# Optimization experiments

Measured on AMD Instinct MI355X. Metric: run time of the kernel, lower is better.

## Reference

```python
import jax, jax.numpy as jnp
import numpy as np

# static config (mirrors init_kwargs)
F_T, S = 8, 24            # video_shape = (F_T, S, S)
K, DIL = 3, 1             # kernel_size, dilation (same for all 3 axes)
HEADS, DHEAD, DIM = 8, 64, 512
INNER = HEADS * DHEAD
PAD = DIL * (K - 1)       # causal: pad 2 at the FRONT of each spatial axis
KJ = K ** 3               # 27 neighbors per query
N_VID = F_T * S * S       # 4608 video tokens


def causal_pad(t):
    # t: [B, D, F, S, S] -> pad front of f/h/w axes (torch F.pad (PAD*?,0) causal layout)
    return jnp.pad(t, ((0, 0), (0, 0), (PAD, 0), (PAD, 0), (PAD, 0)))


def unfold3d(t):
    # torch unfoldNd equivalent. t: [B, D, F+PAD, S+PAD, S+PAD]
    # returns [B, N_VID, KJ, D]; kernel offsets ordered (kf, kh, kw) w fastest,
    # matching torch unfold's channel-major / kernel-minor layout after the
    # rearrange 'b (d j) i -> b i j d'.
    sl = []
    for i in range(K):
        for j in range(K):
            for kk in range(K):
                sl.append(t[:, :, i * DIL:i * DIL + F_T,
                                  j * DIL:j * DIL + S,
                                  kk * DIL:kk * DIL + S])
    u = jnp.stack(sl, axis=2)                      # [B, D, KJ, F, S, S]
    B, D = t.shape[0], t.shape[1]
    u = u.reshape(B, D, KJ, N_VID)
    return jnp.transpose(u, (0, 3, 2, 1))          # [B, N_VID, KJ, D]


def make_mask():
    # True where the neighbor falls into zero padding (out-of-range / future under causal pad)
    ones = jnp.ones((1, 1, F_T, S, S), jnp.float32)
    u = unfold3d(causal_pad(ones))[0, :, :, 0]     # [N_VID, KJ]
    m = u == 0.0
    return jnp.pad(m, ((0, 0), (1, 0)), constant_values=False)  # bos col never masked


def stable_softmax(t, alpha=32.0 ** 2):
    t = t / alpha
    t = t - jax.lax.stop_gradient(jnp.max(t, axis=-1, keepdims=True))
    return jax.nn.softmax(t * alpha, axis=-1)


def setup_inputs() -> dict:
    key = jax.random.key(0)
    ks = jax.random.split(key, 9)
    return {
        "x": jax.random.normal(ks[0], (1, N_VID + 1, DIM), jnp.float32),
        "Wq": jax.random.normal(ks[1], (DIM, INNER), jnp.float32) * 0.02,
        "Wkv": jax.random.normal(ks[2], (DIM, 2 * INNER), jnp.float32) * 0.02,
        "W_th": jax.random.normal(ks[3], (HEADS, HEADS), jnp.float32) * 0.2,
        "Wout": jax.random.normal(ks[4], (INNER, DIM), jnp.float32) * 0.02,
        "bout": jax.random.normal(ks[5], (DIM,), jnp.float32) * 0.02,
        "ax1": jax.random.normal(ks[6], (K, HEADS), jnp.float32),
        "ax2": jax.random.normal(ks[7], (K, HEADS), jnp.float32),
        "ax3": jax.random.normal(ks[8], (K, HEADS), jnp.float32),
    }


def reference(x, Wq, Wkv, W_th, Wout, bout, ax1, ax2, ax3):
    b, n, _ = x.shape                       # b=1, n = 1 + N_VID (no extra padding)
    h, d = HEADS, DHEAD
    scale = d ** -0.5

    q = x @ Wq
    k, v = jnp.split(x @ Wkv, 2, axis=-1)

    def to_heads(t):  # 'b n (h d) -> (b h) n d'
        return t.reshape(b, n, h, d).transpose(0, 2, 1, 3).reshape(b * h, n, d)

    q, k, v = map(to_heads, (q, k, v))
    q = q[:, 1:] * scale                    # drop bos query
    k_bos, v_bos = k[:, :1], v[:, :1]       # [bh, 1, d]
    k, v = k[:, 1:], v[:, 1:]

    def to_vid(t):  # 'b (f h w) d -> b d f h w'
        return t.reshape(b * h, F_T, S, S, d).transpose(0, 4, 1, 2, 3)

    ku = unfold3d(causal_pad(to_vid(k)))    # [bh, N, KJ, d]
    vu = unfold3d(causal_pad(to_vid(v)))
    N = ku.shape[1]

    kb = jnp.broadcast_to(k_bos[:, :, None, :], (b * h, N, 1, d))
    vb = jnp.broadcast_to(v_bos[:, :, None, :], (b * h, N, 1, d))
    ku = jnp.concatenate([kb, ku], axis=2)  # [bh, N, KJ+1, d]
    vu = jnp.concatenate([vb, vu], axis=2)

    sim = jnp.einsum('bid,bijd->bij', q, ku)                 # [bh, N, KJ+1]

    # axial relative position bias over the 3x3x3 kernel, pad 0 for bos column
    rel = (ax1[:, None, None, :] + ax2[None, :, None, :] + ax3[None, None, :, :])
    rel = rel.reshape(KJ, h)                                 # [27, h]
    bias = jnp.pad(rel.T[:, None, :], ((0, 0), (0, 0), (1, 0)))  # [h, 1, KJ+1]

    sim = sim.reshape(b, h, N, KJ + 1) + bias[None]
    mask = make_mask()                                       # [N, KJ+1]
    sim = jnp.where(mask[None, None], -jnp.finfo(sim.dtype).max, sim)

    attn = stable_softmax(sim)                               # [b, h, N, KJ+1]
    attn = jnp.einsum('hg,bgij->bhij', W_th, attn)           # talking heads 1x1 conv

    out = jnp.einsum('bhij,bhijd->bhid', attn, vu.reshape(b, h, N, KJ + 1, d))
    out = jnp.concatenate([v_bos.reshape(b, h, 1, d), out], axis=2)  # re-attach bos value
    out = out.transpose(0, 2, 1, 3).reshape(b, n, h * d)     # '(b h) n d -> b n (h d)'
    return out @ Wout + bout
```

## Files before the change

### kernel.cpp

```cpp
#include <hip/hip_runtime.h>
#include <hip/hip_bf16.h>


constexpr int TFR   = 8;
constexpr int SDIM  = 24;
constexpr int NVID  = TFR * SDIM * SDIM;
constexpr int NTOK  = NVID + 1;
constexpr int NH    = 8;
constexpr int DM    = 512;
constexpr int NJ    = 28;

typedef __attribute__((ext_vector_type(8))) short bf16x8;
typedef __attribute__((ext_vector_type(8))) unsigned short ushort8;
typedef __attribute__((ext_vector_type(4))) float f32x4;

typedef const __attribute__((address_space(1))) unsigned int* gas_ptr;
typedef __attribute__((address_space(3))) unsigned int* las_ptr;

__device__ __forceinline__ float bf2f(unsigned short u) {
    return __uint_as_float((unsigned)u << 16);
}
__device__ __forceinline__ unsigned short f2bf(float f) {
    __hip_bfloat16 h = __float2bfloat16(f);
    return reinterpret_cast<unsigned short&>(h);
}

__global__ __launch_bounds__(256)
void prep_w(const float* __restrict__ Wq, const float* __restrict__ Wkv,
            const float* __restrict__ Wout, const float* __restrict__ x,
            __hip_bfloat16* __restrict__ Wqkvt, __hip_bfloat16* __restrict__ Woutt,
            __hip_bfloat16* __restrict__ xb)
{
    const int tid = threadIdx.x;
    int tb = blockIdx.x;

    if (tb >= 1024) {
        const size_t base = (size_t)(tb - 1024) * 2048 + (size_t)tid * 8;
        if (base < (size_t)NTOK * DM) {
            const float4 f0 = *(const float4*)(x + base);
            const float4 f1 = *(const float4*)(x + base + 4);
            unsigned short v[8] = { f2bf(f0.x), f2bf(f0.y), f2bf(f0.z), f2bf(f0.w),
                                    f2bf(f1.x), f2bf(f1.y), f2bf(f1.z), f2bf(f1.w) };
            *(ushort8*)(xb + base) = *(const ushort8*)v;
        }
        return;
    }

    __shared__ float t[32][33];
    const float* W; __hip_bfloat16* Wt; int Nd, tX, rowOff;
    if (tb < 256)      { W = Wq;   Wt = Wqkvt; Nd = 512;  tX = 16; rowOff = 0;   }
    else if (tb < 768) { tb -= 256; W = Wkv;  Wt = Wqkvt; Nd = 1024; tX = 32; rowOff = 512; }
    else               { tb -= 768; W = Wout; Wt = Woutt; Nd = 512;  tX = 16; rowOff = 0;   }
    const int n0 = (tb % tX) * 32, k0 = (tb / tX) * 32;
    const int r  = tid >> 3;
    const int c4 = (tid & 7) * 4;
    const float4 v = *(const float4*)(W + (size_t)(k0 + r) * Nd + n0 + c4);
    t[r][c4 + 0] = v.x; t[r][c4 + 1] = v.y; t[r][c4 + 2] = v.z; t[r][c4 + 3] = v.w;
    __syncthreads();
    #pragma unroll
    for (int j = 0; j < 4; ++j)
        Wt[(size_t)(rowOff + n0 + r) * 512 + k0 + c4 + j] = __float2bfloat16(t[c4 + j][r]);
}

__global__ __launch_bounds__(256)
void gemm_qkv(const __hip_bfloat16* __restrict__ Ab, const __hip_bfloat16* __restrict__ Bt,
              float* __restrict__ Cq, __hip_bfloat16* __restrict__ Ckv, int M)
{
    constexpr int BM = 128, BN = 128, BK = 64, K = 512;
    __shared__ __align__(16) short As[2][BM * BK];
    __shared__ __align__(16) short Bs[2][BN * BK];

    const int tid  = threadIdx.x;
    const int bid  = blockIdx.x;
    const int xcd  = bid & 7, pos = bid >> 3;
    const int L    = (xcd < 4) ? xcd * 56 + pos : 224 + (xcd - 4) * 55 + pos;
    const int m0   = (L / 12) * BM;
    const int n0   = (L % 12) * BN;

    const int lane = tid & 63;
    const int wave = tid >> 6;
    const int wm   = (wave >> 1) * 64;
    const int wn   = (wave & 1) * 64;
    const int col  = lane & 15;
    const int quad = lane >> 4;

    f32x4 acc[4][4] = {};

    auto stage = [&](int buf, int k0) {
        #pragma unroll
        for (int it = 0; it < 4; ++it) {
            const int idx = it * 256 + tid;
            const int r   = idx >> 3;
            const int u   = (idx & 7) ^ (r & 7);
            const int gm  = (m0 + r < M) ? (m0 + r) : (M - 1);
            const __hip_bfloat16* gp = Ab + (size_t)gm * K + k0 + u * 8;
            __builtin_amdgcn_global_load_lds(
                (gas_ptr)gp, (las_ptr)&As[buf][(it * 256 + wave * 64) * 8], 16, 0, 0);
        }
        #pragma unroll
        for (int it = 0; it < 4; ++it) {
            const int idx = it * 256 + tid;
            const int r   = idx >> 3;
            const int u   = (idx & 7) ^ (r & 7);
            const __hip_bfloat16* gp = Bt + (size_t)(n0 + r) * K + k0 + u * 8;
            __builtin_amdgcn_global_load_lds(
                (gas_ptr)gp, (las_ptr)&Bs[buf][(it * 256 + wave * 64) * 8], 16, 0, 0);
        }
    };

    stage(0, 0);

    #pragma unroll
    for (int t = 0; t < K / BK; ++t) {
        const int cur = t & 1;
        if (t + 1 < K / BK) {
            stage(cur ^ 1, (t + 1) * BK);
            asm volatile("s_waitcnt vmcnt(8)" ::: "memory");
        } else {
            asm volatile("s_waitcnt vmcnt(0)" ::: "memory");
        }
        __builtin_amdgcn_s_barrier();

        #pragma unroll
        for (int ks = 0; ks < 2; ++ks) {
            bf16x8 af[4], bfr[4];
            #pragma unroll
            for (int mt = 0; mt < 4; ++mt) {
                const int r = wm + mt * 16 + col;
                const int u = (ks * 4 + quad) ^ (r & 7);
                af[mt] = *(const bf16x8*)(&As[cur][r * BK + u * 8]);
            }
            #pragma unroll
            for (int nt = 0; nt < 4; ++nt) {
                const int r = wn + nt * 16 + col;
                const int u = (ks * 4 + quad) ^ (r & 7);
                bfr[nt] = *(const bf16x8*)(&Bs[cur][r * BK + u * 8]);
            }
            #pragma unroll
            for (int mt = 0; mt < 4; ++mt)
                #pragma unroll
                for (int nt = 0; nt < 4; ++nt)
                    acc[mt][nt] = __builtin_amdgcn_mfma_f32_16x16x32_bf16(
                        af[mt], bfr[nt], acc[mt][nt], 0, 0, 0);
        }
        __builtin_amdgcn_s_barrier();
    }

    const bool isQ = (n0 < 512);
    #pragma unroll
    for (int mt = 0; mt < 4; ++mt) {
        #pragma unroll
        for (int r = 0; r < 4; ++r) {
            const int row = m0 + wm + mt * 16 + quad * 4 + r;
            if (row >= M) continue;
            #pragma unroll
            for (int nt = 0; nt < 4; ++nt) {
                const int cg = n0 + wn + nt * 16 + col;
                const float v = acc[mt][nt][r];
                if (isQ) Cq[(size_t)row * 512 + cg] = v * 0.125f;
                else     Ckv[(size_t)row * 1024 + (cg - 512)] = __float2bfloat16(v);
            }
        }
    }
}

__global__ __launch_bounds__(256)
void gemm_out(const __hip_bfloat16* __restrict__ A, const __hip_bfloat16* __restrict__ Bt,
              float* __restrict__ C, int M, const float* __restrict__ bias)
{
    constexpr int BM = 64, BN = 64, BK = 64, K = 512;
    __shared__ __align__(16) short As[2][BM * BK];
    __shared__ __align__(16) short Bs[2][BN * BK];

    const int tid  = threadIdx.x;
    const int bid  = blockIdx.x;
    const int L    = (bid & 7) * 73 + (bid >> 3);
    const int m0   = (L >> 3) * BM;
    const int n0   = (L & 7) * BN;
    const int lane = tid & 63;
    const int wave = tid >> 6;
    const int wm   = (wave >> 1) * 32;
    const int wn   = (wave & 1) * 32;
    const int col  = lane & 15;
    const int quad = lane >> 4;

    f32x4 acc[2][2] = {};

    auto stage = [&](int buf, int k0) {
        #pragma unroll
        for (int it = 0; it < 2; ++it) {
            const int idx = it * 256 + tid;
            const int r   = idx >> 3;
            const int u   = (idx & 7) ^ (r & 7);
            const int gm  = (m0 + r < M) ? (m0 + r) : (M - 1);
            const __hip_bfloat16* gp = A + (size_t)gm * K + k0 + u * 8;
            __builtin_amdgcn_global_load_lds(
                (gas_ptr)gp, (las_ptr)&As[buf][(it * 256 + wave * 64) * 8], 16, 0, 0);
        }
        #pragma unroll
        for (int it = 0; it < 2; ++it) {
            const int idx = it * 256 + tid;
            const int r   = idx >> 3;
            const int u   = (idx & 7) ^ (r & 7);
            const __hip_bfloat16* gp = Bt + (size_t)(n0 + r) * K + k0 + u * 8;
            __builtin_amdgcn_global_load_lds(
                (gas_ptr)gp, (las_ptr)&Bs[buf][(it * 256 + wave * 64) * 8], 16, 0, 0);
        }
    };

    stage(0, 0);

    #pragma unroll
    for (int t = 0; t < K / BK; ++t) {
        const int cur = t & 1;
        if (t + 1 < K / BK) {
            stage(cur ^ 1, (t + 1) * BK);
            asm volatile("s_waitcnt vmcnt(4)" ::: "memory");
        } else {
            asm volatile("s_waitcnt vmcnt(0)" ::: "memory");
        }
        __builtin_amdgcn_s_barrier();

        #pragma unroll
        for (int ks = 0; ks < 2; ++ks) {
            bf16x8 af[2], bfr[2];
            #pragma unroll
            for (int mt = 0; mt < 2; ++mt) {
                const int r = wm + mt * 16 + col;
                const int u = (ks * 4 + quad) ^ (r & 7);
                af[mt] = *(const bf16x8*)(&As[cur][r * BK + u * 8]);
            }
            #pragma unroll
            for (int nt = 0; nt < 2; ++nt) {
                const int r = wn + nt * 16 + col;
                const int u = (ks * 4 + quad) ^ (r & 7);
                bfr[nt] = *(const bf16x8*)(&Bs[cur][r * BK + u * 8]);
            }
            #pragma unroll
            for (int mt = 0; mt < 2; ++mt)
                #pragma unroll
                for (int nt = 0; nt < 2; ++nt)
                    acc[mt][nt] = __builtin_amdgcn_mfma_f32_16x16x32_bf16(
                        af[mt], bfr[nt], acc[mt][nt], 0, 0, 0);
        }
        __builtin_amdgcn_s_barrier();
    }

    #pragma unroll
    for (int mt = 0; mt < 2; ++mt) {
        #pragma unroll
        for (int r = 0; r < 4; ++r) {
            const int row = m0 + wm + mt * 16 + quad * 4 + r;
            if (row >= M) continue;
            #pragma unroll
            for (int nt = 0; nt < 2; ++nt) {
                const int cg = n0 + wn + nt * 16 + col;
                C[(size_t)row * 512 + cg] = acc[mt][nt][r] + bias[cg];
            }
        }
    }
}

__device__ __forceinline__ void neigh(int j, int t, int y, int x,
                                      int& row, bool& val,
                                      int& di, int& dj, int& dk)
{
    if (j == 0) { row = 0; val = true; di = 0; dj = 0; dk = 0; return; }
    const int jp = j - 1;
    di = jp / 9; dj = (jp / 3) % 3; dk = jp % 3;
    const int tt = t + di - 2, yy = y + dj - 2, xx = x + dk - 2;
    val = (tt >= 0) && (yy >= 0) && (xx >= 0);
    row = val ? 1 + tt * SDIM * SDIM + yy * SDIM + xx : 0;
}

#define ISSUE_K(B, DST)                                                     \
    { _Pragma("unroll")                                                     \
      for (int u = 0; u < 7; ++u) {                                         \
        int row; bool val; int di, dj, dk;                                  \
        neigh((B) * 7 + u, t, y, x, row, val, di, dj, dk);                  \
        DST[u] = *(const ushort8*)(KVb + (size_t)row * 1024 + lane * 8);    \
      } }

#define DOTS_K(B, SRC)                                                      \
    { _Pragma("unroll")                                                     \
      for (int u = 0; u < 7; ++u) {                                         \
        const int j = (B) * 7 + u;                                          \
        int row; bool val; int di, dj, dk;                                  \
        neigh(j, t, y, x, row, val, di, dj, dk);                            \
        float p = 0.f;                                                      \
        _Pragma("unroll")                                                   \
        for (int e = 0; e < 8; ++e) p += bf2f(SRC[u][e]) * qf[e];           \
        p += __shfl_xor(p, 1);                                              \
        p += __shfl_xor(p, 2);                                              \
        p += __shfl_xor(p, 4);                                              \
        sim[j] = !val ? -1e30f                                              \
               : (j == 0 ? p : p + a1[di] + a2[dj] + a3[dk]);               \
      } }

#define ISSUE_V(B, DST)                                                     \
    { _Pragma("unroll")                                                     \
      for (int u = 0; u < 7; ++u) {                                         \
        int row; bool val; int di, dj, dk;                                  \
        neigh((B) * 7 + u, t, y, x, row, val, di, dj, dk);                  \
        DST[u] = *(const ushort8*)(KVb + (size_t)row * 1024 + 512 + lane * 8); \
      } }

#define ACC_V(B, SRC)                                                       \
    { _Pragma("unroll")                                                     \
      for (int u = 0; u < 7; ++u) {                                         \
        const int j = (B) * 7 + u;                                          \
        const float w = mixed_s[wave][g * NJ + j];                          \
        _Pragma("unroll")                                                   \
        for (int e = 0; e < 8; ++e) acc8[e] += w * bf2f(SRC[u][e]);         \
      } }

__global__ __launch_bounds__(256, 3)
void attn_v5(const float* __restrict__ Q, const __hip_bfloat16* __restrict__ KVb,
             __hip_bfloat16* __restrict__ O,
             const float* __restrict__ W_th,
             const float* __restrict__ ax1, const float* __restrict__ ax2,
             const float* __restrict__ ax3)
{
    __shared__ float attn_s[4][NH * NJ];
    __shared__ float mixed_s[4][NH * NJ];

    const int tid  = threadIdx.x;
    const int wave = tid >> 6;
    const int lane = tid & 63;
    const int g    = lane >> 3;
    const int s    = lane & 7;
    const int bsw  = (blockIdx.x & 7) * (NVID / 4 / 8) + (blockIdx.x >> 3);
    const int i    = __builtin_amdgcn_readfirstlane(bsw * 4 + wave);
    const int qrow = i + 1;

    const int t  = i / (SDIM * SDIM);
    const int rm = i % (SDIM * SDIM);
    const int y  = rm / SDIM;
    const int x  = rm % SDIM;

    float qf[8];
    {
        const float4 q0 = *(const float4*)(Q + (size_t)qrow * DM + lane * 8);
        const float4 q1 = *(const float4*)(Q + (size_t)qrow * DM + lane * 8 + 4);
        qf[0] = q0.x; qf[1] = q0.y; qf[2] = q0.z; qf[3] = q0.w;
        qf[4] = q1.x; qf[5] = q1.y; qf[6] = q1.z; qf[7] = q1.w;
    }
    float a1[3], a2[3], a3[3];
    #pragma unroll
    for (int d = 0; d < 3; ++d) {
        a1[d] = ax1[d * NH + g];
        a2[d] = ax2[d * NH + g];
        a3[d] = ax3[d * NH + g];
    }

    float sim[NJ];
    ushort8 bufA[7], bufB[7];
    ISSUE_K(0, bufA);
    ISSUE_K(1, bufB);
    DOTS_K(0, bufA);
    ISSUE_K(2, bufA);
    DOTS_K(1, bufB);
    ISSUE_K(3, bufB);
    DOTS_K(2, bufA);
    DOTS_K(3, bufB);

    ISSUE_V(0, bufA);

    float m = -1e30f;
    #pragma unroll
    for (int j = 0; j < NJ; ++j) m = fmaxf(m, sim[j]);
    float ssum = 0.f;
    #pragma unroll
    for (int j = 0; j < NJ; ++j) { sim[j] = __expf(sim[j] - m); ssum += sim[j]; }
    const float inv = 1.f / ssum;
    #pragma unroll
    for (int j = 0; j < NJ; ++j) sim[j] *= inv;

    if (s == 0) {
        #pragma unroll
        for (int u = 0; u < 7; ++u) {
            f32x4 v4 = { sim[4*u], sim[4*u+1], sim[4*u+2], sim[4*u+3] };
            *(f32x4*)(&attn_s[wave][g * NJ + 4 * u]) = v4;
        }
    }
    asm volatile("s_waitcnt lgkmcnt(0)" ::: "memory");
    __builtin_amdgcn_s_barrier();

    if (tid < NH * NJ) {
        const int h = tid / NJ, j = tid % NJ;
        #pragma unroll
        for (int q = 0; q < 4; ++q) {
            float acc = 0.f;
            #pragma unroll
            for (int gg = 0; gg < NH; ++gg)
                acc += W_th[h * NH + gg] * attn_s[q][gg * NJ + j];
            mixed_s[q][h * NJ + j] = acc;
        }
    }
    asm volatile("s_waitcnt lgkmcnt(0)" ::: "memory");
    __builtin_amdgcn_s_barrier();

    float acc8[8] = {};
    ISSUE_V(1, bufB);
    ACC_V(0, bufA);
    ISSUE_V(2, bufA);
    ACC_V(1, bufB);
    ISSUE_V(3, bufB);
    ACC_V(2, bufA);
    ACC_V(3, bufB);

    unsigned short o[8];
    #pragma unroll
    for (int e = 0; e < 8; ++e) o[e] = f2bf(acc8[e]);
    *(ushort8*)(O + (size_t)qrow * DM + lane * 8) = *(const ushort8*)o;

    if (i == 0) {
        const ushort8 vb0 = *(const ushort8*)(KVb + 512 + lane * 8);
        *(ushort8*)(O + lane * 8) = vb0;
    }
}

extern "C" void kernel_launch(void* const* d_in, const int* in_sizes, int n_in,
                              void* d_out, int out_size, void* d_ws, size_t ws_size,
                              hipStream_t stream)
{
    const float* x    = (const float*)d_in[0];
    const float* Wq   = (const float*)d_in[1];
    const float* Wkv  = (const float*)d_in[2];
    const float* W_th = (const float*)d_in[3];
    const float* Wout = (const float*)d_in[4];
    const float* bout = (const float*)d_in[5];
    const float* ax1  = (const float*)d_in[6];
    const float* ax2  = (const float*)d_in[7];
    const float* ax3  = (const float*)d_in[8];
    float* out = (float*)d_out;

    char* p = (char*)d_ws;
    float* Qf = (float*)p;                       p += (size_t)NTOK * DM * 4;
    __hip_bfloat16* KVb   = (__hip_bfloat16*)p;  p += (size_t)NTOK * 2 * DM * 2;
    __hip_bfloat16* Ob    = (__hip_bfloat16*)p;  p += (size_t)NTOK * DM * 2;
    __hip_bfloat16* Wqkvt = (__hip_bfloat16*)p;  p += (size_t)3 * DM * DM * 2;
    __hip_bfloat16* Woutt = (__hip_bfloat16*)p;  p += (size_t)DM * DM * 2;
    __hip_bfloat16* xb    = (__hip_bfloat16*)p;  p += (size_t)NTOK * DM * 2;

    const dim3 blk(256);

    prep_w<<<2177, blk, 0, stream>>>(Wq, Wkv, Wout, x, Wqkvt, Woutt, xb);

    gemm_qkv<<<444, blk, 0, stream>>>(xb, Wqkvt, Qf, KVb, NTOK);

    attn_v5<<<dim3(NVID / 4), blk, 0, stream>>>(Qf, KVb, Ob, W_th, ax1, ax2, ax3);

    gemm_out<<<584, blk, 0, stream>>>(Ob, Woutt, out, NTOK, bout);
}
```

Before: 121.9 us.

## Process two adjacent queries per wave sharing overlapping neighbor K/V loads

Each wave now handles two x-adjacent query tokens. It loads 4 consecutive K/V rows per (dt,dy) group instead of 3 per query, so the two overlapping 3x3x3 neighborhoods share loads and global traffic in the attention stage drops. The grid is halved to 576 blocks, with doubled shared buffers and two softmax/accumulator sets per wave. This raises register pressure, which may limit occupancy, and leaves fewer blocks to fill the machine.

Result: slower. 145.0 us (+19.0%).

```diff
diff --git a/kernel.cpp b/kernel.cpp
--- a/kernel.cpp
+++ b/kernel.cpp
@@ -261,89 +261,87 @@
     }
 }
 
-__device__ __forceinline__ void neigh(int j, int t, int y, int x,
-                                      int& row, bool& val,
-                                      int& di, int& dj, int& dk)
-{
-    if (j == 0) { row = 0; val = true; di = 0; dj = 0; dk = 0; return; }
-    const int jp = j - 1;
-    di = jp / 9; dj = (jp / 3) % 3; dk = jp % 3;
-    const int tt = t + di - 2, yy = y + dj - 2, xx = x + dk - 2;
-    val = (tt >= 0) && (yy >= 0) && (xx >= 0);
-    row = val ? 1 + tt * SDIM * SDIM + yy * SDIM + xx : 0;
-}
-
-#define ISSUE_K(B, DST)                                                     \
-    { _Pragma("unroll")                                                     \
-      for (int u = 0; u < 7; ++u) {                                         \
-        int row; bool val; int di, dj, dk;                                  \
-        neigh((B) * 7 + u, t, y, x, row, val, di, dj, dk);                  \
-        DST[u] = *(const ushort8*)(KVb + (size_t)row * 1024 + lane * 8);    \
+#define ISSUE_G(G, DST, OFF)                                                \
+    { const int di = (G) / 3, dj = (G) % 3;                                 \
+      const int tt = t + di - 2, yy = y + dj - 2;                           \
+      _Pragma("unroll")                                                     \
+      for (int e = 0; e < 4; ++e) {                                         \
+        const int xx = x0 - 2 + e;                                          \
+        const bool v = (tt >= 0) && (yy >= 0) && (xx >= 0);                 \
+        const int row = v ? 1 + tt * SDIM * SDIM + yy * SDIM + xx : 0;      \
+        DST[e] = *(const ushort8*)(KVb + (size_t)row * 1024 + (OFF) + lane * 8); \
       } }
 
-#define DOTS_K(B, SRC)                                                      \
-    { _Pragma("unroll")                                                     \
-      for (int u = 0; u < 7; ++u) {                                         \
-        const int j = (B) * 7 + u;                                          \
-        int row; bool val; int di, dj, dk;                                  \
-        neigh(j, t, y, x, row, val, di, dj, dk);                            \
-        float p = 0.f;                                                      \
+#define DOTS_G(G, SRC)                                                      \
+    { const int di = (G) / 3, dj = (G) % 3;                                 \
+      const int tt = t + di - 2, yy = y + dj - 2;                           \
+      const bool pv = (tt >= 0) && (yy >= 0);                               \
+      _Pragma("unroll")                                                     \
+      for (int dk = 0; dk < 3; ++dk) {                                      \
+        const int j = 1 + (G) * 3 + dk;                                     \
+        const float bias = a1[di] + a2[dj] + a3[dk];                        \
+        float p0 = 0.f, p1 = 0.f;                                           \
         _Pragma("unroll")                                                   \
-        for (int e = 0; e < 8; ++e) p += bf2f(SRC[u][e]) * qf[e];           \
-        p += __shfl_xor(p, 1);                                              \
-        p += __shfl_xor(p, 2);                                              \
-        p += __shfl_xor(p, 4);                                              \
-        sim[j] = !val ? -1e30f                                              \
-               : (j == 0 ? p : p + a1[di] + a2[dj] + a3[dk]);               \
+        for (int e = 0; e < 8; ++e) {                                       \
+          p0 += bf2f(SRC[dk][e])     * qf0[e];                              \
+          p1 += bf2f(SRC[dk + 1][e]) * qf1[e];                              \
+        }                                                                   \
+        p0 += __shfl_xor(p0, 1); p0 += __shfl_xor(p0, 2); p0 += __shfl_xor(p0, 4); \
+        p1 += __shfl_xor(p1, 1); p1 += __shfl_xor(p1, 2); p1 += __shfl_xor(p1, 4); \
+        sim0[j] = (pv && (x0 - 2 + dk >= 0)) ? p0 + bias : -1e30f;          \
+        sim1[j] = (pv && (x0 - 1 + dk >= 0)) ? p1 + bias : -1e30f;          \
       } }
 
-#define ISSUE_V(B, DST)                                                     \
-    { _Pragma("unroll")                                                     \
-      for (int u = 0; u < 7; ++u) {                                         \
-        int row; bool val; int di, dj, dk;                                  \
-        neigh((B) * 7 + u, t, y, x, row, val, di, dj, dk);                  \
-        DST[u] = *(const ushort8*)(KVb + (size_t)row * 1024 + 512 + lane * 8); \
+#define ACC_G(G, SRC)                                                       \
+    { const int di = (G) / 3, dj = (G) % 3;                                 \
+      const int tt = t + di - 2, yy = y + dj - 2;                           \
+      const bool pv = (tt >= 0) && (yy >= 0);                               \
+      _Pragma("unroll")                                                     \
+      for (int dk = 0; dk < 3; ++dk) {                                      \
+        const int j = 1 + (G) * 3 + dk;                                     \
+        const float w0 = (pv && (x0 - 2 + dk >= 0)) ? mx0[j] : 0.f;         \
+        const float w1 = (pv && (x0 - 1 + dk >= 0)) ? mx1[j] : 0.f;         \
+        _Pragma("unroll")                                                   \
+        for (int e = 0; e < 8; ++e) {                                       \
+          acc0[e] += w0 * bf2f(SRC[dk][e]);                                 \
+          acc1[e] += w1 * bf2f(SRC[dk + 1][e]);                             \
+        }                                                                   \
       } }
 
-#define ACC_V(B, SRC)                                                       \
-    { _Pragma("unroll")                                                     \
-      for (int u = 0; u < 7; ++u) {                                         \
-        const int j = (B) * 7 + u;                                          \
-        const float w = mixed_s[wave][g * NJ + j];                          \
-        _Pragma("unroll")                                                   \
-        for (int e = 0; e < 8; ++e) acc8[e] += w * bf2f(SRC[u][e]);         \
-      } }
-
 __global__ __launch_bounds__(256, 3)
-void attn_v5(const float* __restrict__ Q, const __hip_bfloat16* __restrict__ KVb,
+void attn_v6(const float* __restrict__ Q, const __hip_bfloat16* __restrict__ KVb,
              __hip_bfloat16* __restrict__ O,
              const float* __restrict__ W_th,
              const float* __restrict__ ax1, const float* __restrict__ ax2,
              const float* __restrict__ ax3)
 {
-    __shared__ float attn_s[4][NH * NJ];
-    __shared__ float mixed_s[4][NH * NJ];
+    __shared__ float attn_s[8][NH * NJ];
+    __shared__ float mixed_s[8][NH * NJ];
 
     const int tid  = threadIdx.x;
     const int wave = tid >> 6;
     const int lane = tid & 63;
     const int g    = lane >> 3;
     const int s    = lane & 7;
-    const int bsw  = (blockIdx.x & 7) * (NVID / 4 / 8) + (blockIdx.x >> 3);
-    const int i    = __builtin_amdgcn_readfirstlane(bsw * 4 + wave);
-    const int qrow = i + 1;
-
-    const int t  = i / (SDIM * SDIM);
-    const int rm = i % (SDIM * SDIM);
+    const int bsw  = (blockIdx.x & 7) * (576 / 8) + (blockIdx.x >> 3);
+    const int q0   = __builtin_amdgcn_readfirstlane(bsw * 8 + wave * 2);
+    const int q1   = q0 + 1;
+
+    const int t  = q0 / (SDIM * SDIM);
+    const int rm = q0 % (SDIM * SDIM);
     const int y  = rm / SDIM;
-    const int x  = rm % SDIM;
-
-    float qf[8];
+    const int x0 = rm % SDIM;
+
+    float qf0[8], qf1[8];
     {
-        const float4 q0 = *(const float4*)(Q + (size_t)qrow * DM + lane * 8);
-        const float4 q1 = *(const float4*)(Q + (size_t)qrow * DM + lane * 8 + 4);
-        qf[0] = q0.x; qf[1] = q0.y; qf[2] = q0.z; qf[3] = q0.w;
-        qf[4] = q1.x; qf[5] = q1.y; qf[6] = q1.z; qf[7] = q1.w;
+        const float4 a = *(const float4*)(Q + (size_t)(q0 + 1) * DM + lane * 8);
+        const float4 b = *(const float4*)(Q + (size_t)(q0 + 1) * DM + lane * 8 + 4);
+        qf0[0] = a.x; qf0[1] = a.y; qf0[2] = a.z; qf0[3] = a.w;
+        qf0[4] = b.x; qf0[5] = b.y; qf0[6] = b.z; qf0[7] = b.w;
+        const float4 c = *(const float4*)(Q + (size_t)(q1 + 1) * DM + lane * 8);
+        const float4 d = *(const float4*)(Q + (size_t)(q1 + 1) * DM + lane * 8 + 4);
+        qf1[0] = c.x; qf1[1] = c.y; qf1[2] = c.z; qf1[3] = c.w;
+        qf1[4] = d.x; qf1[5] = d.y; qf1[6] = d.z; qf1[7] = d.w;
     }
     float a1[3], a2[3], a3[3];
     #pragma unroll
@@ -353,34 +351,55 @@
         a3[d] = ax3[d * NH + g];
     }
 
-    float sim[NJ];
-    ushort8 bufA[7], bufB[7];
-    ISSUE_K(0, bufA);
-    ISSUE_K(1, bufB);
-    DOTS_K(0, bufA);
-    ISSUE_K(2, bufA);
-    DOTS_K(1, bufB);
-    ISSUE_K(3, bufB);
-    DOTS_K(2, bufA);
-    DOTS_K(3, bufB);
-
-    ISSUE_V(0, bufA);
-
-    float m = -1e30f;
-    #pragma unroll
-    for (int j = 0; j < NJ; ++j) m = fmaxf(m, sim[j]);
-    float ssum = 0.f;
-    #pragma unroll
-    for (int j = 0; j < NJ; ++j) { sim[j] = __expf(sim[j] - m); ssum += sim[j]; }
-    const float inv = 1.f / ssum;
-    #pragma unroll
-    for (int j = 0; j < NJ; ++j) sim[j] *= inv;
+    float sim0[NJ], sim1[NJ];
+    ushort8 bufA[4], bufB[4];
+    ushort8 kbos = *(const ushort8*)(KVb + lane * 8);
+    ISSUE_G(0, bufA, 0);
+    ISSUE_G(1, bufB, 0);
+    {
+        float p0 = 0.f, p1 = 0.f;
+        #pragma unroll
+        for (int e = 0; e < 8; ++e) {
+            p0 += bf2f(kbos[e]) * qf0[e];
+            p1 += bf2f(kbos[e]) * qf1[e];
+        }
+        p0 += __shfl_xor(p0, 1); p0 += __shfl_xor(p0, 2); p0 += __shfl_xor(p0, 4);
+        p1 += __shfl_xor(p1, 1); p1 += __shfl_xor(p1, 2); p1 += __shfl_xor(p1, 4);
+        sim0[0] = p0; sim1[0] = p1;
+    }
+    DOTS_G(0, bufA);  ISSUE_G(2, bufA, 0);
+    DOTS_G(1, bufB);  ISSUE_G(3, bufB, 0);
+    DOTS_G(2, bufA);  ISSUE_G(4, bufA, 0);
+    DOTS_G(3, bufB);  ISSUE_G(5, bufB, 0);
+    DOTS_G(4, bufA);  ISSUE_G(6, bufA, 0);
+    DOTS_G(5, bufB);  ISSUE_G(7, bufB, 0);
+    DOTS_G(6, bufA);  ISSUE_G(8, bufA, 0);
+    DOTS_G(7, bufB);
+    DOTS_G(8, bufA);
+
+    ushort8 vbos = *(const ushort8*)(KVb + 512 + lane * 8);
+    ISSUE_G(0, bufB, 512);
+
+    float m0 = -1e30f, m1 = -1e30f;
+    #pragma unroll
+    for (int j = 0; j < NJ; ++j) { m0 = fmaxf(m0, sim0[j]); m1 = fmaxf(m1, sim1[j]); }
+    float ss0 = 0.f, ss1 = 0.f;
+    #pragma unroll
+    for (int j = 0; j < NJ; ++j) {
+        sim0[j] = __expf(sim0[j] - m0); ss0 += sim0[j];
+        sim1[j] = __expf(sim1[j] - m1); ss1 += sim1[j];
+    }
+    const float iv0 = 1.f / ss0, iv1 = 1.f / ss1;
+    #pragma unroll
+    for (int j = 0; j < NJ; ++j) { sim0[j] *= iv0; sim1[j] *= iv1; }
 
     if (s == 0) {
         #pragma unroll
         for (int u = 0; u < 7; ++u) {
-            f32x4 v4 = { sim[4*u], sim[4*u+1], sim[4*u+2], sim[4*u+3] };
-            *(f32x4*)(&attn_s[wave][g * NJ + 4 * u]) = v4;
+            f32x4 v0 = { sim0[4*u], sim0[4*u+1], sim0[4*u+2], sim0[4*u+3] };
+            f32x4 v1 = { sim1[4*u], sim1[4*u+1], sim1[4*u+2], sim1[4*u+3] };
+            *(f32x4*)(&attn_s[wave * 2 + 0][g * NJ + 4 * u]) = v0;
+            *(f32x4*)(&attn_s[wave * 2 + 1][g * NJ + 4 * u]) = v1;
         }
     }
     asm volatile("s_waitcnt lgkmcnt(0)" ::: "memory");
@@ -389,7 +408,7 @@
     if (tid < NH * NJ) {
         const int h = tid / NJ, j = tid % NJ;
         #pragma unroll
-        for (int q = 0; q < 4; ++q) {
+        for (int q = 0; q < 8; ++q) {
             float acc = 0.f;
             #pragma unroll
             for (int gg = 0; gg < NH; ++gg)
@@ -400,23 +419,39 @@
     asm volatile("s_waitcnt lgkmcnt(0)" ::: "memory");
     __builtin_amdgcn_s_barrier();
 
-    float acc8[8] = {};
-    ISSUE_V(1, bufB);
-    ACC_V(0, bufA);
-    ISSUE_V(2, bufA);
-    ACC_V(1, bufB);
-    ISSUE_V(3, bufB);
-    ACC_V(2, bufA);
-    ACC_V(3, bufB);
-
-    unsigned short o[8];
-    #pragma unroll
-    for (int e = 0; e < 8; ++e) o[e] = f2bf(acc8[e]);
-    *(ushort8*)(O + (size_t)qrow * DM + lane * 8) = *(const ushort8*)o;
-
-    if (i == 0) {
-        const ushort8 vb0 = *(const ushort8*)(KVb + 512 + lane * 8);
-        *(ushort8*)(O + lane * 8) = vb0;
+    const float* mx0 = &mixed_s[wave * 2 + 0][g * NJ];
+    const float* mx1 = &mixed_s[wave * 2 + 1][g * NJ];
+    float acc0[8] = {}, acc1[8] = {};
+    {
+        const float w0 = mx0[0], w1 = mx1[0];
+        #pragma unroll
+        for (int e = 0; e < 8; ++e) {
+            acc0[e] += w0 * bf2f(vbos[e]);
+            acc1[e] += w1 * bf2f(vbos[e]);
+        }
+    }
+    ISSUE_G(1, bufA, 512);
+    ACC_G(0, bufB);  ISSUE_G(2, bufB, 512);
+    ACC_G(1, bufA);  ISSUE_G(3, bufA, 512);
+    ACC_G(2, bufB);  ISSUE_G(4, bufB, 512);
+    ACC_G(3, bufA);  ISSUE_G(5, bufA, 512);
+    ACC_G(4, bufB);  ISSUE_G(6, bufB, 512);
+    ACC_G(5, bufA);  ISSUE_G(7, bufA, 512);
+    ACC_G(6, bufB);  ISSUE_G(8, bufB, 512);
+    ACC_G(7, bufA);
+    ACC_G(8, bufB);
+
+    unsigned short o0[8], o1[8];
+    #pragma unroll
+    for (int e = 0; e < 8; ++e) { o0[e] = f2bf(acc0[e]); o1[e] = f2bf(acc1[e]); }
+    *(ushort8*)(O + (size_t)(q0 + 1) * DM + lane * 8) = *(const ushort8*)o0;
+    *(ushort8*)(O + (size_t)(q1 + 1) * DM + lane * 8) = *(const ushort8*)o1;
+
+    if (q0 == 0) {
+        unsigned short ob[8];
+        #pragma unroll
+        for (int e = 0; e < 8; ++e) ob[e] = (unsigned short)vbos[e];
+        *(ushort8*)(O + lane * 8) = *(const ushort8*)ob;
     }
 }
 
@@ -449,7 +484,7 @@
 
     gemm_qkv<<<444, blk, 0, stream>>>(xb, Wqkvt, Qf, KVb, NTOK);
 
-    attn_v5<<<dim3(NVID / 4), blk, 0, stream>>>(Qf, KVb, Ob, W_th, ax1, ax2, ax3);
+    attn_v6<<<576, blk, 0, stream>>>(Qf, KVb, Ob, W_th, ax1, ax2, ax3);
 
     gemm_out<<<584, blk, 0, stream>>>(Ob, Woutt, out, NTOK, bout);
 }
```
